# Kernel optimization log

Hardware: AMD Instinct MI355X
Metric: run time of the kernel (lower is better)

Reference implementation:

```python
import jax, jax.numpy as jnp
import numpy as np

TOP_K = 4  # num_experts_per_tok


def setup_inputs() -> dict:
    key = jax.random.key(0)
    ks = jax.random.split(key, 8)
    B, S, H, E, F = 1, 2048, 2048, 16, 1408
    Fs = 2 * F  # shared expert intermediate = moe_intermediate_size * n_shared_experts
    s = 0.02  # weight init scale for sane numerics
    return {
        "hidden_states": jax.random.normal(ks[0], (B, S, H), jnp.float32),
        "gate_weight": jax.random.normal(ks[1], (E, H), jnp.float32) * s,
        "w_gate": jax.random.normal(ks[2], (E, H, F), jnp.float32) * s,
        "w_up": jax.random.normal(ks[3], (E, H, F), jnp.float32) * s,
        "w_down": jax.random.normal(ks[4], (E, F, H), jnp.float32) * s,
        "ws_gate": jax.random.normal(ks[5], (H, Fs), jnp.float32) * s,
        "ws_up": jax.random.normal(ks[6], (H, Fs), jnp.float32) * s,
        "ws_down": jax.random.normal(ks[7], (Fs, H), jnp.float32) * s,
    }


def reference(hidden_states, gate_weight, w_gate, w_up, w_down, ws_gate, ws_up, ws_down):
    B, S, H = hidden_states.shape
    E = gate_weight.shape[0]
    x = hidden_states.reshape(-1, H)  # [T, H]
    T = x.shape[0]

    # --- gate: fp32 linear, softmax over experts, top-k, scatter to dense mask ---
    logits = jnp.einsum("th,eh->te", x.astype(jnp.float32), gate_weight.astype(jnp.float32))
    probs = jax.nn.softmax(logits, axis=1)
    top_vals, top_idx = jax.lax.top_k(probs, TOP_K)  # [T, K]
    # dense routing weights [T, E]; scatter_add of top-k softmax values (no renorm)
    dense_w = jnp.zeros((T, E), probs.dtype).at[jnp.arange(T)[:, None], top_idx].add(top_vals)

    # --- routed experts: gated SiLU MLP per expert, weighted combine ---
    g = jnp.einsum("th,ehf->tef", x, w_gate)
    u = jnp.einsum("th,ehf->tef", x, w_up)
    a = jax.nn.silu(g) * u  # [T, E, F]
    # fold expert combine into the down projection to avoid a [T, E, H] intermediate
    routed = jnp.einsum("te,tef,efh->th", dense_w.astype(x.dtype), a, w_down)

    # --- shared expert on identity path ---
    shared = jnp.einsum("tf,fh->th", jax.nn.silu(x @ ws_gate) * (x @ ws_up), ws_down)

    out = (routed + shared).reshape(B, S, H)
    return out
```

## Files before the change

kernel.cpp:

```cpp
#include <hip/hip_runtime.h>

#define TT 2048
#define HD 2048
#define FD 1408
#define NE 16
#define NG 18

typedef __attribute__((ext_vector_type(4))) float f32x4;
typedef __attribute__((ext_vector_type(8))) short short8;
typedef __attribute__((ext_vector_type(8))) __bf16 bf16x8;
typedef __attribute__((ext_vector_type(4))) unsigned short u16x4;
typedef __attribute__((ext_vector_type(8))) unsigned short u16x8;
typedef __attribute__((ext_vector_type(2))) unsigned int u32x2;

__device__ __forceinline__ unsigned short f2bf(float f) {
  unsigned u = __builtin_bit_cast(unsigned, f);
  u += 0x7fffu + ((u >> 16) & 1u);
  return (unsigned short)(u >> 16);
}
__device__ __forceinline__ unsigned pack2(float lo, float hi) {
  return (unsigned)f2bf(lo) | ((unsigned)f2bf(hi) << 16);
}

template <typename T>
__device__ __forceinline__ auto mfma_try(T a, T b, f32x4 c, int)
    -> decltype(__builtin_amdgcn_mfma_f32_16x16x32_bf16(a, b, c, 0, 0, 0)) {
  return __builtin_amdgcn_mfma_f32_16x16x32_bf16(a, b, c, 0, 0, 0);
}
template <typename T, typename BV = bf16x8>
__device__ __forceinline__ f32x4 mfma_try(T a, T b, f32x4 c, long) {
  BV aa = __builtin_bit_cast(BV, a);
  BV bb = __builtin_bit_cast(BV, b);
  return __builtin_amdgcn_mfma_f32_16x16x32_bf16(aa, bb, c, 0, 0, 0);
}
__device__ __forceinline__ f32x4 mfma16(short8 a, short8 b, f32x4 c) {
  return mfma_try(a, b, c, 0);
}

__device__ __forceinline__ void gload16(const void* g, void* l) {
  __builtin_amdgcn_global_load_lds(
      (const __attribute__((address_space(1))) void*)g,
      (__attribute__((address_space(3))) void*)l, 16, 0, 0);
}

#define CB1 (FD / 64)
#define CB2 (HD / 128)
#define MAXW1 2464
#define MAXW2 1792

__global__ void gate_kernel(const float* __restrict__ x, const float* __restrict__ gw,
                            float* __restrict__ dense_w) {
  int wid = threadIdx.x >> 6;
  int lane = threadIdx.x & 63;
  int t = blockIdx.x * 4 + wid;
  if (t >= TT) return;
  const float* xr = x + (size_t)t * HD;
  float acc[NE];
#pragma unroll
  for (int e = 0; e < NE; ++e) acc[e] = 0.f;
  for (int h = lane; h < HD; h += 64) {
    float xv = xr[h];
#pragma unroll
    for (int e = 0; e < NE; ++e) acc[e] += xv * gw[e * HD + h];
  }
#pragma unroll
  for (int e = 0; e < NE; ++e) {
    float v = acc[e];
#pragma unroll
    for (int s = 32; s > 0; s >>= 1) v += __shfl_xor(v, s, 64);
    acc[e] = v;
  }
  float mx = acc[0];
#pragma unroll
  for (int e = 1; e < NE; ++e) mx = fmaxf(mx, acc[e]);
  float p[NE]; float sum = 0.f;
#pragma unroll
  for (int e = 0; e < NE; ++e) { p[e] = __expf(acc[e] - mx); sum += p[e]; }
  float inv = 1.f / sum;
#pragma unroll
  for (int e = 0; e < NE; ++e) p[e] *= inv;
  unsigned chosen = 0;
#pragma unroll
  for (int k = 0; k < 4; ++k) {
    int bi = 0; float bv = -1.f;
#pragma unroll
    for (int e = 0; e < NE; ++e) {
      bool ok = !((chosen >> e) & 1) && (p[e] > bv);
      bv = ok ? p[e] : bv;
      bi = ok ? e : bi;
    }
    chosen |= 1u << bi;
  }
  if (lane < NE)
    dense_w[t * NE + lane] = ((chosen >> lane) & 1) ? p[lane] : 0.f;
}

__global__ void build_lists(const float* __restrict__ dense_w, int* __restrict__ tok,
                            float* __restrict__ scale, int* __restrict__ counts) {
  int g = blockIdx.x;
  int lane = threadIdx.x;
  if (g >= NE) {
    for (int i = lane; i < TT; i += 64) { tok[g * TT + i] = i; scale[g * TT + i] = 1.f; }
    if (lane == 0) counts[g] = TT;
    return;
  }
  int base = 0;
  for (int c0 = 0; c0 < TT; c0 += 64) {
    int t = c0 + lane;
    float w = dense_w[t * NE + g];
    bool pred = w > 0.f;
    unsigned long long b = __ballot(pred);
    if (pred) {
      int pos = base + __popcll(b & ((1ull << lane) - 1ull));
      tok[g * TT + pos] = t;
      scale[g * TT + pos] = w;
    }
    base += __popcll(b);
  }
  if (lane == 0) counts[g] = base;
}

__global__ void prefix_kernel(const int* __restrict__ counts, int* __restrict__ rowOff,
                              int* __restrict__ work1, int* __restrict__ work2,
                              int* __restrict__ meta) {
  const int tid = threadIdx.x;
  auto NRB = [&](int g) { return (counts[g] + 127) >> 7; };
  if (tid == 0) {
    int s = 0;
    for (int g = 0; g < NE; ++g) { rowOff[g] = s; s += counts[g]; }
    rowOff[16] = 4 * TT;
    rowOff[17] = 4 * TT + TT;
    int n1 = 0, n2 = 0;
    for (int g = 0; g < NG; ++g) { n1 += NRB(g) * CB1; n2 += NRB(g) * CB2; }
    meta[0] = n1; meta[1] = (n1 + 7) / 8;
    meta[2] = n2; meta[3] = (n2 + 7) / 8;
  }
  if (tid < NG * CB1) {
    int g = tid / CB1, cb = tid % CB1;
    int base = 0;
    for (int gg = 0; gg < g; ++gg) base += NRB(gg) * CB1;
    int n = NRB(g);
    base += cb * n;
    for (int r = 0; r < n; ++r) work1[base + r] = (g << 16) | (cb << 8) | r;
  }
  if (tid < NG * CB2) {
    int g = tid / CB2, cb = tid % CB2;
    int base = 0;
    for (int gg = 0; gg < g; ++gg) base += NRB(gg) * CB2;
    int n = NRB(g);
    base += cb * n;
    for (int r = 0; r < n; ++r) work2[base + r] = (g << 16) | (cb << 8) | r;
  }
}

__global__ void cvt_bf16_kernel(const float* __restrict__ in,
                                unsigned short* __restrict__ out, int n4) {
  int i = blockIdx.x * blockDim.x + threadIdx.x;
  if (i < n4) {
    f32x4 v = ((const f32x4*)in)[i];
    u16x4 h;
    h.x = f2bf(v.x); h.y = f2bf(v.y); h.z = f2bf(v.z); h.w = f2bf(v.w);
    ((u16x4*)out)[i] = h;
  }
}

__global__ __launch_bounds__(256, 4) void gemm1_v8(
    const unsigned short* __restrict__ xb,
    const float* __restrict__ w_gate, const float* __restrict__ w_up,
    const float* __restrict__ ws_gate, const float* __restrict__ ws_up,
    const int* __restrict__ tok, const float* __restrict__ scale,
    const int* __restrict__ counts, const int* __restrict__ rowOff,
    const int* __restrict__ work, const int* __restrict__ meta,
    unsigned short* __restrict__ Abuf) {
  const int nw = meta[0], per = meta[1];
  const int xcd = blockIdx.x & 7, slot = blockIdx.x >> 3;
  if (slot >= per) return;
  const int w = xcd * per + slot;
  if (w >= nw) return;
  const int e = work[w];
  const int g = e >> 16, cb = (e >> 8) & 255, rb = e & 255;
  const int count = counts[g];

  __shared__ __align__(16) unsigned short sA[2][128 * 32];
  __shared__ __align__(16) unsigned short sG[2][64 * 32];
  __shared__ __align__(16) unsigned short sU[2][64 * 32];

  const int tid = threadIdx.x, lane = tid & 63, wid = tid >> 6;
  const int wr = (wid >> 1) * 64, wc = (wid & 1) * 32;

  const int lr = lane >> 2, lc = lane & 3;
  const int ra0 = wid * 32 + lr, ra1 = wid * 32 + 16 + lr;
  int gi0 = rb * 128 + ra0, gi1 = rb * 128 + ra1;
  int t0 = (gi0 < count) ? tok[g * TT + gi0] : 0;
  int t1 = (gi1 < count) ? tok[g * TT + gi1] : 0;
  const unsigned short* aG0 = xb + (size_t)t0 * HD + ((lc ^ ((ra0 >> 1) & 3)) * 8);
  const unsigned short* aG1 = xb + (size_t)t1 * HD + ((lc ^ ((ra1 >> 1) & 3)) * 8);

  const int kp = tid >> 4, n0 = (tid & 15) * 4;
  const float *Bg, *Bu; size_t ldb; int bcol0;
  if (g < NE) {
    size_t o = (size_t)g * HD * FD;
    Bg = w_gate + o; Bu = w_up + o; ldb = FD; bcol0 = cb * 64;
  } else {
    Bg = ws_gate; Bu = ws_up; ldb = 2 * FD; bcol0 = (g - NE) * FD + cb * 64;
  }
  const float* gp = Bg + (size_t)(2 * kp) * ldb + bcol0 + n0;
  const float* up = Bu + (size_t)(2 * kp) * ldb + bcol0 + n0;
  int bwi[4];
#pragma unroll
  for (int j = 0; j < 4; ++j) {
    int n = n0 + j;
    bwi[j] = n * 16 + (((kp >> 2) ^ ((n >> 2) & 3)) << 2) + (kp & 3);
  }

  const f32x4 fz = {0.f, 0.f, 0.f, 0.f};
  f32x4 accg[4][2], accu[4][2];
#pragma unroll
  for (int m = 0; m < 4; ++m)
#pragma unroll
    for (int n = 0; n < 2; ++n) { accg[m][n] = fz; accu[m][n] = fz; }

  f32x4 g0, g1, u0, u1;

  auto STAGEA = [&](int bu, int s) {
    size_t ko = (size_t)s * 32;
    gload16(aG0 + ko, &sA[bu][wid * 1024]);
    gload16(aG1 + ko, &sA[bu][wid * 1024 + 512]);
  };
  auto LOADB = [&](int s) {
    const float* _g = gp + (size_t)s * 32 * ldb;
    const float* _u = up + (size_t)s * 32 * ldb;
    g0 = *(const f32x4*)_g; g1 = *(const f32x4*)(_g + ldb);
    u0 = *(const f32x4*)_u; u1 = *(const f32x4*)(_u + ldb);
  };
  auto STOREB = [&](int bu) {
    unsigned* gw_ = (unsigned*)sG[bu];
    unsigned* uw_ = (unsigned*)sU[bu];
#pragma unroll
    for (int j = 0; j < 4; ++j) {
      gw_[bwi[j]] = pack2(g0[j], g1[j]);
      uw_[bwi[j]] = pack2(u0[j], u1[j]);
    }
  };

  auto COMPUTE = [&](int bu) {
    const int ksel = lane >> 4;
    short8 av[4], bg[2], bv[2];
#pragma unroll
    for (int n = 0; n < 2; ++n) {
      int c = wc + n * 16 + (lane & 15);
      int idx = c * 32 + ((ksel ^ ((c >> 2) & 3)) << 3);
      bg[n] = *(const short8*)&sG[bu][idx];
      bv[n] = *(const short8*)&sU[bu][idx];
    }
#pragma unroll
    for (int m = 0; m < 4; ++m) {
      int r = wr + m * 16 + (lane & 15);
      av[m] = *(const short8*)&sA[bu][r * 32 + ((ksel ^ ((r >> 1) & 3)) << 3)];
    }
#pragma unroll
    for (int m = 0; m < 4; ++m)
#pragma unroll
      for (int n = 0; n < 2; ++n) {
        accg[m][n] = mfma16(av[m], bg[n], accg[m][n]);
        accu[m][n] = mfma16(av[m], bv[n], accu[m][n]);
      }
  };

  const int NK = HD / 32;
  LOADB(0);
  STAGEA(0, 0);
  STOREB(0);
  LOADB(1);
  __syncthreads();
#pragma unroll 1
  for (int s = 0; s < NK; ++s) {
    int bu = s & 1;
    if (s + 1 < NK) STAGEA(bu ^ 1, s + 1);
    COMPUTE(bu);
    if (s + 1 < NK) STOREB(bu ^ 1);
    if (s + 2 < NK) LOADB(s + 2);
    __syncthreads();
  }

  const int rowBase = rowOff[g] + rb * 128;
#pragma unroll
  for (int m = 0; m < 4; ++m)
#pragma unroll
    for (int r = 0; r < 4; ++r) {
      int rl = wr + m * 16 + ((lane >> 4) << 2) + r;
      int gi = rb * 128 + rl;
      if (gi < count) {
        float sc = scale[g * TT + gi];
#pragma unroll
        for (int n = 0; n < 2; ++n) {
          int cl = wc + n * 16 + (lane & 15);
          float gv = accg[m][n][r], uv = accu[m][n][r];
          float a = gv / (1.f + __expf(-gv)) * uv * sc;
          Abuf[(size_t)(rowBase + rl) * FD + cb * 64 + cl] = f2bf(a);
        }
      }
    }
}

__global__ __launch_bounds__(256, 4) void gemm2_v8(
    const unsigned short* __restrict__ Abuf,
    const float* __restrict__ w_down, const float* __restrict__ ws_down,
    const int* __restrict__ tok, const int* __restrict__ counts,
    const int* __restrict__ rowOff, const int* __restrict__ work,
    const int* __restrict__ meta, float* __restrict__ out) {
  const int nw = meta[2], per = meta[3];
  const int xcd = blockIdx.x & 7, slot = blockIdx.x >> 3;
  if (slot >= per) return;
  const int w = xcd * per + slot;
  if (w >= nw) return;
  const int e = work[w];
  const int g = e >> 16, cb = (e >> 8) & 255, rb = e & 255;
  const int count = counts[g];

  __shared__ __align__(16) unsigned short sA[2][128 * 32];
  __shared__ __align__(16) unsigned short sB[2][128 * 32];

  const int tid = threadIdx.x, lane = tid & 63, wid = tid >> 6;
  const int wr = (wid >> 1) * 64, wc = (wid & 1) * 64;

  const int rowBase = rowOff[g] + rb * 128;

  const int lr = lane >> 2, lc = lane & 3;
  const int ra0 = wid * 32 + lr, ra1 = wid * 32 + 16 + lr;
  const unsigned short* aG0 =
      Abuf + (size_t)(rowBase + ra0) * FD + ((lc ^ ((ra0 >> 1) & 3)) * 8);
  const unsigned short* aG1 =
      Abuf + (size_t)(rowBase + ra1) * FD + ((lc ^ ((ra1 >> 1) & 3)) * 8);

  const int kg = tid >> 5, n0 = (tid & 31) * 4;
  const float* bp;
  if (g < NE)
    bp = w_down + (size_t)g * FD * HD + (size_t)(4 * kg) * HD + cb * 128 + n0;
  else
    bp = ws_down + (size_t)((g - NE) * FD + 4 * kg) * HD + cb * 128 + n0;
  int bwi[4];
#pragma unroll
  for (int j = 0; j < 4; ++j) {
    int n = n0 + j;
    bwi[j] = n * 16 + (((kg >> 1) ^ ((n >> 2) & 3)) << 2) + ((2 * kg) & 3);
  }

  const f32x4 fz = {0.f, 0.f, 0.f, 0.f};
  f32x4 acc[4][4];
#pragma unroll
  for (int m = 0; m < 4; ++m)
#pragma unroll
    for (int n = 0; n < 4; ++n) acc[m][n] = fz;

  f32x4 b0, b1, b2, b3;

  auto STAGEA = [&](int bu, int s) {
    size_t ko = (size_t)s * 32;
    gload16(aG0 + ko, &sA[bu][wid * 1024]);
    gload16(aG1 + ko, &sA[bu][wid * 1024 + 512]);
  };
  auto LOADB = [&](int s) {
    const float* _b = bp + (size_t)s * 32 * HD;
    b0 = *(const f32x4*)_b;
    b1 = *(const f32x4*)(_b + HD);
    b2 = *(const f32x4*)(_b + 2 * HD);
    b3 = *(const f32x4*)(_b + 3 * HD);
  };
  auto STOREB = [&](int bu) {
    unsigned* bw_ = (unsigned*)sB[bu];
#pragma unroll
    for (int j = 0; j < 4; ++j) {
      u32x2 v;
      v.x = pack2(b0[j], b1[j]);
      v.y = pack2(b2[j], b3[j]);
      *(u32x2*)&bw_[bwi[j]] = v;
    }
  };

  auto COMPUTE = [&](int bu) {
    const int ksel = lane >> 4;
    short8 av[4], bv[4];
#pragma unroll
    for (int n = 0; n < 4; ++n) {
      int c = wc + n * 16 + (lane & 15);
      bv[n] = *(const short8*)&sB[bu][c * 32 + ((ksel ^ ((c >> 2) & 3)) << 3)];
    }
#pragma unroll
    for (int m = 0; m < 4; ++m) {
      int r = wr + m * 16 + (lane & 15);
      av[m] = *(const short8*)&sA[bu][r * 32 + ((ksel ^ ((r >> 1) & 3)) << 3)];
    }
#pragma unroll
    for (int m = 0; m < 4; ++m)
#pragma unroll
      for (int n = 0; n < 4; ++n) acc[m][n] = mfma16(av[m], bv[n], acc[m][n]);
  };

  const int NK = FD / 32;
  LOADB(0);
  STAGEA(0, 0);
  STOREB(0);
  LOADB(1);
  __syncthreads();
#pragma unroll 1
  for (int s = 0; s < NK; ++s) {
    int bu = s & 1;
    if (s + 1 < NK) STAGEA(bu ^ 1, s + 1);
    COMPUTE(bu);
    if (s + 1 < NK) STOREB(bu ^ 1);
    if (s + 2 < NK) LOADB(s + 2);
    __syncthreads();
  }

#pragma unroll
  for (int m = 0; m < 4; ++m)
#pragma unroll
    for (int r = 0; r < 4; ++r) {
      int rl = wr + m * 16 + ((lane >> 4) << 2) + r;
      int gi = rb * 128 + rl;
      if (gi < count) {
        int t = tok[g * TT + gi];
        float* op = out + (size_t)t * HD + cb * 128;
#pragma unroll
        for (int n = 0; n < 4; ++n)
          atomicAdd(op + wc + n * 16 + (lane & 15), acc[m][n][r]);
      }
    }
}

extern "C" void kernel_launch(void* const* d_in, const int* in_sizes, int n_in,
                              void* d_out, int out_size, void* d_ws, size_t ws_size,
                              hipStream_t stream) {
  const float* x      = (const float*)d_in[0];
  const float* gw     = (const float*)d_in[1];
  const float* w_gate = (const float*)d_in[2];
  const float* w_up   = (const float*)d_in[3];
  const float* w_down = (const float*)d_in[4];
  const float* wsg    = (const float*)d_in[5];
  const float* wsu    = (const float*)d_in[6];
  const float* wsd    = (const float*)d_in[7];
  float* out = (float*)d_out;

  char* ws = (char*)d_ws;
  float* dense_w = (float*)(ws);
  int*   tok     = (int*)(ws + (140 << 10));
  float* scale   = (float*)(ws + (290 << 10));
  int*   counts  = (int*)(ws + (440 << 10));
  int*   rowOff  = (int*)(ws + (441 << 10));
  int*   work1   = (int*)(ws + (444 << 10));
  int*   work2   = (int*)(ws + (456 << 10));
  int*   meta    = (int*)(ws + (464 << 10));
  unsigned short* Abuf = (unsigned short*)(ws + (1ull  << 20));
  unsigned short* xb   = (unsigned short*)(ws + (36ull << 20));

  hipMemsetAsync(d_out, 0, (size_t)out_size * sizeof(float), stream);
  gate_kernel<<<TT / 4, 256, 0, stream>>>(x, gw, dense_w);
  build_lists<<<NG, 64, 0, stream>>>(dense_w, tok, scale, counts);
  prefix_kernel<<<1, 512, 0, stream>>>(counts, rowOff, work1, work2, meta);
  cvt_bf16_kernel<<<(TT * HD / 4 + 255) / 256, 256, 0, stream>>>(x, xb, TT * HD / 4);

  gemm1_v8<<<MAXW1, 256, 0, stream>>>(
      xb, w_gate, w_up, wsg, wsu, tok, scale, counts, rowOff, work1, meta, Abuf);
  gemm2_v8<<<MAXW2, 256, 0, stream>>>(
      Abuf, w_down, wsd, tok, counts, rowOff, work2, meta, out);
}
```

Before: 510.4 us.

## Use packed bf16 convert, k-major swizzled B tiles, and reorder loads before compute

```diff
diff --git a/kernel.cpp b/kernel.cpp
--- a/kernel.cpp
+++ b/kernel.cpp
@@ -11,15 +11,17 @@
 typedef __attribute__((ext_vector_type(8))) __bf16 bf16x8;
 typedef __attribute__((ext_vector_type(4))) unsigned short u16x4;
 typedef __attribute__((ext_vector_type(8))) unsigned short u16x8;
-typedef __attribute__((ext_vector_type(2))) unsigned int u32x2;
+typedef __attribute__((ext_vector_type(4))) unsigned int u32x4;
 
 __device__ __forceinline__ unsigned short f2bf(float f) {
   unsigned u = __builtin_bit_cast(unsigned, f);
   u += 0x7fffu + ((u >> 16) & 1u);
   return (unsigned short)(u >> 16);
 }
-__device__ __forceinline__ unsigned pack2(float lo, float hi) {
-  return (unsigned)f2bf(lo) | ((unsigned)f2bf(hi) << 16);
+__device__ __forceinline__ unsigned cvt_pk(float lo, float hi) {
+  unsigned r;
+  asm("v_cvt_pk_bf16_f32 %0, %1, %2" : "=v"(r) : "v"(lo), "v"(hi));
+  return r;
 }
 
 template <typename T>
@@ -164,7 +166,7 @@
   }
 }
 
-__global__ __launch_bounds__(256, 4) void gemm1_v8(
+__global__ __launch_bounds__(256, 4) void gemm1_v9(
     const unsigned short* __restrict__ xb,
     const float* __restrict__ w_gate, const float* __restrict__ w_up,
     const float* __restrict__ ws_gate, const float* __restrict__ ws_up,
@@ -182,8 +184,8 @@
   const int count = counts[g];
 
   __shared__ __align__(16) unsigned short sA[2][128 * 32];
-  __shared__ __align__(16) unsigned short sG[2][64 * 32];
-  __shared__ __align__(16) unsigned short sU[2][64 * 32];
+  __shared__ __align__(16) unsigned sG[2][16 * 64];
+  __shared__ __align__(16) unsigned sU[2][16 * 64];
 
   const int tid = threadIdx.x, lane = tid & 63, wid = tid >> 6;
   const int wr = (wid >> 1) * 64, wc = (wid & 1) * 32;
@@ -196,7 +198,7 @@
   const unsigned short* aG0 = xb + (size_t)t0 * HD + ((lc ^ ((ra0 >> 1) & 3)) * 8);
   const unsigned short* aG1 = xb + (size_t)t1 * HD + ((lc ^ ((ra1 >> 1) & 3)) * 8);
 
-  const int kp = tid >> 4, n0 = (tid & 15) * 4;
+  const int kp = tid >> 4, nq = tid & 15;
   const float *Bg, *Bu; size_t ldb; int bcol0;
   if (g < NE) {
     size_t o = (size_t)g * HD * FD;
@@ -204,14 +206,9 @@
   } else {
     Bg = ws_gate; Bu = ws_up; ldb = 2 * FD; bcol0 = (g - NE) * FD + cb * 64;
   }
-  const float* gp = Bg + (size_t)(2 * kp) * ldb + bcol0 + n0;
-  const float* up = Bu + (size_t)(2 * kp) * ldb + bcol0 + n0;
-  int bwi[4];
-#pragma unroll
-  for (int j = 0; j < 4; ++j) {
-    int n = n0 + j;
-    bwi[j] = n * 16 + (((kp >> 2) ^ ((n >> 2) & 3)) << 2) + (kp & 3);
-  }
+  const float* gp = Bg + (size_t)(2 * kp) * ldb + bcol0 + nq * 4;
+  const float* up = Bu + (size_t)(2 * kp) * ldb + bcol0 + nq * 4;
+  const int bwa = kp * 64 + (((nq ^ kp) & 15) << 2);
 
   const f32x4 fz = {0.f, 0.f, 0.f, 0.f};
   f32x4 accg[4][2], accu[4][2];
@@ -234,13 +231,14 @@
     u0 = *(const f32x4*)_u; u1 = *(const f32x4*)(_u + ldb);
   };
   auto STOREB = [&](int bu) {
-    unsigned* gw_ = (unsigned*)sG[bu];
-    unsigned* uw_ = (unsigned*)sU[bu];
+    u32x4 wg_, wu_;
 #pragma unroll
     for (int j = 0; j < 4; ++j) {
-      gw_[bwi[j]] = pack2(g0[j], g1[j]);
-      uw_[bwi[j]] = pack2(u0[j], u1[j]);
-    }
+      wg_[j] = cvt_pk(g0[j], g1[j]);
+      wu_[j] = cvt_pk(u0[j], u1[j]);
+    }
+    *(u32x4*)&sG[bu][bwa] = wg_;
+    *(u32x4*)&sU[bu][bwa] = wu_;
   };
 
   auto COMPUTE = [&](int bu) {
@@ -248,10 +246,18 @@
     short8 av[4], bg[2], bv[2];
 #pragma unroll
     for (int n = 0; n < 2; ++n) {
-      int c = wc + n * 16 + (lane & 15);
-      int idx = c * 32 + ((ksel ^ ((c >> 2) & 3)) << 3);
-      bg[n] = *(const short8*)&sG[bu][idx];
-      bv[n] = *(const short8*)&sU[bu][idx];
+      int cc = wc + n * 16 + (lane & 15);
+      int ch = cc >> 2, cm = cc & 3;
+      u32x4 tg, tu;
+#pragma unroll
+      for (int i = 0; i < 4; ++i) {
+        int kpp = 4 * ksel + i;
+        int idx = kpp * 64 + (((ch ^ kpp) & 15) << 2) + cm;
+        tg[i] = sG[bu][idx];
+        tu[i] = sU[bu][idx];
+      }
+      bg[n] = __builtin_bit_cast(short8, tg);
+      bv[n] = __builtin_bit_cast(short8, tu);
     }
 #pragma unroll
     for (int m = 0; m < 4; ++m) {
@@ -276,10 +282,12 @@
 #pragma unroll 1
   for (int s = 0; s < NK; ++s) {
     int bu = s & 1;
-    if (s + 1 < NK) STAGEA(bu ^ 1, s + 1);
+    if (s + 1 < NK) {
+      STAGEA(bu ^ 1, s + 1);
+      STOREB(bu ^ 1);
+    }
+    if (s + 2 < NK) LOADB(s + 2);
     COMPUTE(bu);
-    if (s + 1 < NK) STOREB(bu ^ 1);
-    if (s + 2 < NK) LOADB(s + 2);
     __syncthreads();
   }
 
@@ -303,7 +311,7 @@
     }
 }
 
-__global__ __launch_bounds__(256, 4) void gemm2_v8(
+__global__ __launch_bounds__(256, 4) void gemm2_v9(
     const unsigned short* __restrict__ Abuf,
     const float* __restrict__ w_down, const float* __restrict__ ws_down,
     const int* __restrict__ tok, const int* __restrict__ counts,
@@ -319,7 +327,7 @@
   const int count = counts[g];
 
   __shared__ __align__(16) unsigned short sA[2][128 * 32];
-  __shared__ __align__(16) unsigned short sB[2][128 * 32];
+  __shared__ __align__(16) unsigned sB[2][16 * 128];
 
   const int tid = threadIdx.x, lane = tid & 63, wid = tid >> 6;
   const int wr = (wid >> 1) * 64, wc = (wid & 1) * 64;
@@ -333,18 +341,15 @@
   const unsigned short* aG1 =
       Abuf + (size_t)(rowBase + ra1) * FD + ((lc ^ ((ra1 >> 1) & 3)) * 8);
 
-  const int kg = tid >> 5, n0 = (tid & 31) * 4;
+  const int kg = tid >> 5, nq = tid & 31;
   const float* bp;
   if (g < NE)
-    bp = w_down + (size_t)g * FD * HD + (size_t)(4 * kg) * HD + cb * 128 + n0;
+    bp = w_down + (size_t)g * FD * HD + (size_t)(4 * kg) * HD + cb * 128 + nq * 4;
   else
-    bp = ws_down + (size_t)((g - NE) * FD + 4 * kg) * HD + cb * 128 + n0;
-  int bwi[4];
-#pragma unroll
-  for (int j = 0; j < 4; ++j) {
-    int n = n0 + j;
-    bwi[j] = n * 16 + (((kg >> 1) ^ ((n >> 2) & 3)) << 2) + ((2 * kg) & 3);
-  }
+    bp = ws_down + (size_t)((g - NE) * FD + 4 * kg) * HD + cb * 128 + nq * 4;
+  const int kp0 = 2 * kg, kp1 = 2 * kg + 1;
+  const int bwa0 = kp0 * 128 + (((nq ^ kp0) & 31) << 2);
+  const int bwa1 = kp1 * 128 + (((nq ^ kp1) & 31) << 2);
 
   const f32x4 fz = {0.f, 0.f, 0.f, 0.f};
   f32x4 acc[4][4];
@@ -368,14 +373,14 @@
     b3 = *(const f32x4*)(_b + 3 * HD);
   };
   auto STOREB = [&](int bu) {
-    unsigned* bw_ = (unsigned*)sB[bu];
+    u32x4 w0, w1;
 #pragma unroll
     for (int j = 0; j < 4; ++j) {
-      u32x2 v;
-      v.x = pack2(b0[j], b1[j]);
-      v.y = pack2(b2[j], b3[j]);
-      *(u32x2*)&bw_[bwi[j]] = v;
-    }
+      w0[j] = cvt_pk(b0[j], b1[j]);
+      w1[j] = cvt_pk(b2[j], b3[j]);
+    }
+    *(u32x4*)&sB[bu][bwa0] = w0;
+    *(u32x4*)&sB[bu][bwa1] = w1;
   };
 
   auto COMPUTE = [&](int bu) {
@@ -383,8 +388,15 @@
     short8 av[4], bv[4];
 #pragma unroll
     for (int n = 0; n < 4; ++n) {
-      int c = wc + n * 16 + (lane & 15);
-      bv[n] = *(const short8*)&sB[bu][c * 32 + ((ksel ^ ((c >> 2) & 3)) << 3)];
+      int cc = wc + n * 16 + (lane & 15);
+      int ch = cc >> 2, cm = cc & 3;
+      u32x4 tb;
+#pragma unroll
+      for (int i = 0; i < 4; ++i) {
+        int kpp = 4 * ksel + i;
+        tb[i] = sB[bu][kpp * 128 + (((ch ^ kpp) & 31) << 2) + cm];
+      }
+      bv[n] = __builtin_bit_cast(short8, tb);
     }
 #pragma unroll
     for (int m = 0; m < 4; ++m) {
@@ -406,10 +418,12 @@
 #pragma unroll 1
   for (int s = 0; s < NK; ++s) {
     int bu = s & 1;
-    if (s + 1 < NK) STAGEA(bu ^ 1, s + 1);
+    if (s + 1 < NK) {
+      STAGEA(bu ^ 1, s + 1);
+      STOREB(bu ^ 1);
+    }
+    if (s + 2 < NK) LOADB(s + 2);
     COMPUTE(bu);
-    if (s + 1 < NK) STOREB(bu ^ 1);
-    if (s + 2 < NK) LOADB(s + 2);
     __syncthreads();
   }
 
@@ -460,8 +474,8 @@
   prefix_kernel<<<1, 512, 0, stream>>>(counts, rowOff, work1, work2, meta);
   cvt_bf16_kernel<<<(TT * HD / 4 + 255) / 256, 256, 0, stream>>>(x, xb, TT * HD / 4);
 
-  gemm1_v8<<<MAXW1, 256, 0, stream>>>(
+  gemm1_v9<<<MAXW1, 256, 0, stream>>>(
       xb, w_gate, w_up, wsg, wsu, tok, scale, counts, rowOff, work1, meta, Abuf);
-  gemm2_v8<<<MAXW2, 256, 0, stream>>>(
+  gemm2_v9<<<MAXW2, 256, 0, stream>>>(
       Abuf, w_down, wsd, tok, counts, rowOff, work2, meta, out);
 }
```

After: 578.2 us. +13.3%, slower.
